# Optimization experiments

Measured on AMD Instinct MI355X. Metric: run time of the kernel, lower is better.

Reference implementation:

```python
import jax, jax.numpy as jnp
import numpy as np

B, I, O, G = 4096, 256, 256, 8
GRID_MIN, GRID_MAX, RHO = -2.0, 2.0, 1.0


def setup_inputs() -> dict:
    key = jax.random.key(0)
    ks = jax.random.split(key, 8)
    return {
        "x_re": jax.random.normal(ks[0], (B, I), dtype=jnp.float32),
        "x_im": jax.random.normal(ks[1], (B, I), dtype=jnp.float32),
        "realweights": jax.random.normal(ks[2], (I, O, G, G), dtype=jnp.float32),
        "complexweights": jax.random.normal(ks[3], (I, O, G, G), dtype=jnp.float32),
        "silu_weight_re": jax.random.normal(ks[4], (I, O), dtype=jnp.float32),
        "silu_weight_im": jax.random.normal(ks[5], (I, O), dtype=jnp.float32),
        "silu_bias_re": 0.1 * jax.random.normal(ks[6], (I, O), dtype=jnp.float32),
        "silu_bias_im": 0.1 * jax.random.normal(ks[7], (I, O), dtype=jnp.float32),
    }


def reference(x_re, x_im, realweights, complexweights,
              silu_weight_re, silu_weight_im, silu_bias_re, silu_bias_im):
    # Complex grid: grid[u, v] = lin[u] + i * lin[v]
    lin = jnp.linspace(GRID_MIN, GRID_MAX, G, dtype=x_re.dtype)
    # |x - grid|^2 = (x_re - lin_u)^2 + (x_im - lin_v)^2  -> (B, I, G, G)
    dre = x_re[:, :, None, None] - lin[None, None, :, None]
    dim = x_im[:, :, None, None] - lin[None, None, None, :]
    basis = jnp.exp(-(dre * dre + dim * dim) / RHO)  # real-valued (B, I, G, G)
    # RBF contraction: real and imaginary output channels
    out_re = jnp.einsum('biuv,iouv->bo', basis, realweights)
    out_im = jnp.einsum('biuv,iouv->bo', basis, complexweights)
    # Complex SiLU (complex_weight variant): silu applied component-wise,
    # then complex-multiplied by silu_weight, plus bias, summed over i.
    s_re = jax.nn.silu(x_re)  # (B, I)
    s_im = jax.nn.silu(x_im)
    out_re = out_re + s_re @ silu_weight_re - s_im @ silu_weight_im + jnp.sum(silu_bias_re, axis=0)
    out_im = out_im + s_im @ silu_weight_re + s_re @ silu_weight_im + jnp.sum(silu_bias_im, axis=0)
    # Return complex output as stacked (real, imag): (B, O, 2)
    return jnp.stack([out_re, out_im], axis=-1)
```

## Files before the change

### kernel.cpp

```cpp
#include <hip/hip_runtime.h>
#include <stdint.h>

typedef float floatx4 __attribute__((ext_vector_type(4)));
typedef _Float16 half8 __attribute__((ext_vector_type(8)));
typedef _Float16 half2t __attribute__((ext_vector_type(2)));

constexpr int I_SZ = 256, O_SZ = 256, NCOL = 512, B_SZ = 4096;
constexpr int KSTEPS = 264;
constexpr float GSTEP = 4.0f / 7.0f;
constexpr float NLOG2E = -1.44269504088896f;

__device__ __forceinline__ float silu_f(float a) {
  return a * __builtin_amdgcn_rcpf(1.f + __builtin_amdgcn_exp2f(a * NLOG2E));
}
__device__ __forceinline__ void gload_lds16(const void* g, void* l) {
  __builtin_amdgcn_global_load_lds((const __attribute__((address_space(1))) void*)g,
                                   (__attribute__((address_space(3))) void*)l,
                                   16, 0, 0);
}

union H8 { half8 v; half2t h[4]; uint32_t u[4]; };

__global__ void prelude(const float* __restrict__ rw, const float* __restrict__ cw,
                        const float* __restrict__ swre, const float* __restrict__ swim,
                        const float* __restrict__ bre, const float* __restrict__ bim,
                        const float* __restrict__ xre, const float* __restrict__ xim,
                        _Float16* __restrict__ wpack, float* __restrict__ bsum,
                        _Float16* __restrict__ eivT, _Float16* __restrict__ erqT,
                        _Float16* __restrict__ sTab, float* __restrict__ out) {
  __shared__ float tileR[64][65];
  __shared__ float tileI[64][65];
  const int bid = blockIdx.x, tid = threadIdx.x;

  if (bid < 4224) {
    int idx = bid * 256 + tid;
    int kb = idx >> 12;
    int rem = idx & 4095;
    int n = rem >> 3, gp = rem & 7;
    int g = gp ^ (n & 7);
    int o = n >> 1, c = n & 1;
    float w[8];
    if (kb < 256) {
      const float* W = (c ? cw : rw) + (((size_t)kb * O_SZ + o) << 6) + (g << 3);
      float4 a = *(const float4*)W;
      float4 b = *(const float4*)(W + 4);
      w[0] = a.x; w[1] = a.y; w[2] = a.z; w[3] = a.w;
      w[4] = b.x; w[5] = b.y; w[6] = b.z; w[7] = b.w;
    } else {
      int kp0 = ((kb - 256) << 6) + (g << 3);
      #pragma unroll
      for (int e = 0; e < 8; ++e) {
        int kp = kp0 + e, i = kp >> 1, ci = kp & 1;
        float a = swre[i * O_SZ + o], b = swim[i * O_SZ + o];
        w[e] = (c == 0) ? (ci == 0 ? a : -b) : (ci == 0 ? b : a);
      }
    }
    H8 val;
    #pragma unroll
    for (int e = 0; e < 8; ++e) val.v[e] = (_Float16)w[e];
    *(H8*)(wpack + (size_t)idx * 8) = val;
  } else if (bid < 4480) {
    int tb = bid - 4224;
    int bt = tb & 63, it = tb >> 6;
    int b0 = bt << 6, i0 = it << 6;
    int il = tid & 63, bh = tid >> 6;
    #pragma unroll
    for (int k = 0; k < 16; ++k) {
      int bl = bh + (k << 2);
      tileR[bl][il] = xre[(size_t)(b0 + bl) * I_SZ + i0 + il];
      tileI[bl][il] = xim[(size_t)(b0 + bl) * I_SZ + i0 + il];
    }
    __syncthreads();
    #pragma unroll
    for (int k = 0; k < 16; ++k) {
      int p = k * 256 + tid;
      int i_l = p >> 6, b_l = p & 63;
      float xr = tileR[b_l][i_l];
      float xi = tileI[b_l][i_l];
      float eru[8], eiv[8];
      #pragma unroll
      for (int g = 0; g < 8; ++g) {
        float dr = xr - (-2.0f + g * GSTEP);
        float di = xi - (-2.0f + g * GSTEP);
        eru[g] = __builtin_amdgcn_exp2f(dr * dr * NLOG2E);
        eiv[g] = __builtin_amdgcn_exp2f(di * di * NLOG2E);
      }
      size_t base = ((size_t)(i0 + i_l) * B_SZ + b0 + b_l) * 8;
      H8 ev, eq;
      #pragma unroll
      for (int g = 0; g < 8; ++g) ev.v[g] = (_Float16)eiv[g];
      #pragma unroll
      for (int q = 0; q < 4; ++q) { eq.v[2 * q] = (_Float16)eru[q]; eq.v[2 * q + 1] = (_Float16)eru[q + 4]; }
      *(H8*)(eivT + base) = ev;
      *(H8*)(erqT + base) = eq;
    }
  } else if (bid < 4992) {
    int tg = (bid - 4480) * 256 + tid;
    int b = tg >> 5, io = (tg & 31) << 3;
    const float* pr = xre + (size_t)b * I_SZ + io;
    const float* pi = xim + (size_t)b * I_SZ + io;
    float4 r0 = *(const float4*)pr, r1 = *(const float4*)(pr + 4);
    float4 q0 = *(const float4*)pi, q1 = *(const float4*)(pi + 4);
    H8 lo, hi;
    lo.v[0] = (_Float16)silu_f(r0.x); lo.v[1] = (_Float16)silu_f(q0.x);
    lo.v[2] = (_Float16)silu_f(r0.y); lo.v[3] = (_Float16)silu_f(q0.y);
    lo.v[4] = (_Float16)silu_f(r0.z); lo.v[5] = (_Float16)silu_f(q0.z);
    lo.v[6] = (_Float16)silu_f(r0.w); lo.v[7] = (_Float16)silu_f(q0.w);
    hi.v[0] = (_Float16)silu_f(r1.x); hi.v[1] = (_Float16)silu_f(q1.x);
    hi.v[2] = (_Float16)silu_f(r1.y); hi.v[3] = (_Float16)silu_f(q1.y);
    hi.v[4] = (_Float16)silu_f(r1.z); hi.v[5] = (_Float16)silu_f(q1.z);
    hi.v[6] = (_Float16)silu_f(r1.w); hi.v[7] = (_Float16)silu_f(q1.w);
    _Float16* dst = sTab + (size_t)b * 512 + 2 * io;
    *(H8*)dst = lo;
    *(H8*)(dst + 8) = hi;
  } else if (bid < 5120) {
    int w = tid >> 6, l = tid & 63;
    int n = (bid - 4992) * 4 + w;
    int o = n >> 1;
    const float* src = ((n & 1) ? bim : bre) + o;
    float s = 0.f;
    #pragma unroll
    for (int a = 0; a < 4; ++a) s += src[(size_t)(a * 64 + l) * O_SZ];
    #pragma unroll
    for (int off = 32; off; off >>= 1) s += __shfl_down(s, off, 64);
    if (l == 0) bsum[n] = s;
  } else {
    int z = bid - 5120;
    float4* o4 = (float4*)out;
    float4 zv = {0.f, 0.f, 0.f, 0.f};
    #pragma unroll
    for (int k = 0; k < 4; ++k) o4[(size_t)z * 1024 + k * 256 + tid] = zv;
  }
}

__global__ __launch_bounds__(256, 2) void cvkan_gemm(
    const _Float16* __restrict__ eivT, const _Float16* __restrict__ erqT,
    const _Float16* __restrict__ sTab,
    const _Float16* __restrict__ wpack, const float* __restrict__ bsum,
    float* __restrict__ out) {
  __shared__ __align__(16) _Float16 Bs[2][64 * 64];

  const int tid = threadIdx.x, bid = blockIdx.x;
  const int kch = bid & 7;
  const int rest = bid >> 3;
  const int mt = rest & 7, nt = rest >> 3;
  const int b0 = mt * 512, n0 = nt * 64;
  const int w = tid >> 6, l = tid & 63;
  const int lm = l & 15, q = l >> 4;
  const int row0 = b0 + w * 128 + lm;

  floatx4 acc[8][4] = {};

  {
    const _Float16* slab = wpack + ((size_t)(kch * 32) * NCOL + n0) * 64 + (w << 10) + (l << 3);
    _Float16* dst = &Bs[0][0] + (w << 10);
    gload_lds16(slab, dst);
    gload_lds16(slab + 512, dst + 512);
  }

  for (int j = 0; j < 33; ++j) {
    const int s = (j < 32) ? (kch * 32 + j) : (256 + kch);

    __syncthreads();

    half8 eivr[8]; half2t erqr[8];
    half8 afs[8][2];
    if (j < 32) {
      #pragma unroll
      for (int mm = 0; mm < 8; ++mm) {
        size_t base = ((size_t)s * B_SZ + row0 + mm * 16) * 8;
        eivr[mm] = *(const half8*)(eivT + base);
        erqr[mm] = *(const half2t*)(erqT + base + (q << 1));
      }
    } else {
      #pragma unroll
      for (int mm = 0; mm < 8; ++mm) {
        const _Float16* p = sTab + (size_t)(row0 + mm * 16) * 512 + kch * 64 + (q << 3);
        afs[mm][0] = *(const half8*)p;
        afs[mm][1] = *(const half8*)(p + 32);
      }
    }

    if (j < 32) {
      const int s1 = (j < 31) ? (s + 1) : (256 + kch);
      const _Float16* slab = wpack + ((size_t)s1 * NCOL + n0) * 64 + (w << 10) + (l << 3);
      _Float16* dst = &Bs[(j + 1) & 1][0] + (w << 10);
      gload_lds16(slab, dst);
      gload_lds16(slab + 512, dst + 512);
    }

    half8 bf[4][2];
    const _Float16* bp0 = &Bs[j & 1][0];
    #pragma unroll
    for (int nn = 0; nn < 4; ++nn) {
      int c = nn * 16 + lm;
      const _Float16* bp = bp0 + (c << 6);
      bf[nn][0] = *(const half8*)(bp + ((q       ^ (c & 7)) << 3));
      bf[nn][1] = *(const half8*)(bp + (((q + 4) ^ (c & 7)) << 3));
    }

    #pragma unroll
    for (int mm = 0; mm < 8; ++mm) {
      half8 a0, a1;
      if (j < 32) {
        H8 ev; ev.v = eivr[mm];
        half2t e0 = {erqr[mm].x, erqr[mm].x};
        half2t e1 = {erqr[mm].y, erqr[mm].y};
        H8 r0, r1;
        #pragma unroll
        for (int t = 0; t < 4; ++t) { r0.h[t] = e0 * ev.h[t]; r1.h[t] = e1 * ev.h[t]; }
        a0 = r0.v; a1 = r1.v;
      } else {
        a0 = afs[mm][0]; a1 = afs[mm][1];
      }
      #pragma unroll
      for (int nn = 0; nn < 4; ++nn) {
        acc[mm][nn] = __builtin_amdgcn_mfma_f32_16x16x32_f16(a0, bf[nn][0], acc[mm][nn], 0, 0, 0);
        acc[mm][nn] = __builtin_amdgcn_mfma_f32_16x16x32_f16(a1, bf[nn][1], acc[mm][nn], 0, 0, 0);
      }
    }
  }

  #pragma unroll
  for (int nn = 0; nn < 4; ++nn) {
    int col = n0 + nn * 16 + lm;
    float bv = (kch == 7) ? bsum[col] : 0.0f;
    #pragma unroll
    for (int mm = 0; mm < 8; ++mm) {
      int r0 = b0 + w * 128 + mm * 16 + (q << 2);
      #pragma unroll
      for (int r2 = 0; r2 < 4; ++r2)
        atomicAdd(out + (size_t)(r0 + r2) * NCOL + col, acc[mm][nn][r2] + bv);
    }
  }
}

extern "C" void kernel_launch(void* const* d_in, const int* in_sizes, int n_in,
                              void* d_out, int out_size, void* d_ws, size_t ws_size,
                              hipStream_t stream) {
  const float* xre  = (const float*)d_in[0];
  const float* xim  = (const float*)d_in[1];
  const float* rw   = (const float*)d_in[2];
  const float* cw   = (const float*)d_in[3];
  const float* swre = (const float*)d_in[4];
  const float* swim = (const float*)d_in[5];
  const float* bre  = (const float*)d_in[6];
  const float* bim  = (const float*)d_in[7];
  float* out = (float*)d_out;

  size_t off = 0;
  _Float16* wpack = (_Float16*)((char*)d_ws + off); off += (size_t)KSTEPS * NCOL * 64 * 2;
  _Float16* eivT  = (_Float16*)((char*)d_ws + off); off += (size_t)I_SZ * B_SZ * 8 * 2;
  _Float16* erqT  = (_Float16*)((char*)d_ws + off); off += (size_t)I_SZ * B_SZ * 8 * 2;
  _Float16* sTab  = (_Float16*)((char*)d_ws + off); off += (size_t)B_SZ * 512 * 2;
  float*    bsum  = (float*)((char*)d_ws + off);

  prelude<<<5632, 256, 0, stream>>>(rw, cw, swre, swim, bre, bim, xre, xim,
                                    wpack, bsum, eivT, erqT, sTab, out);
  cvkan_gemm<<<512, 256, 0, stream>>>(eivT, erqT, sTab, wpack, bsum, out);
}
```

Measured before the change: 233.0 us.

## Software-pipeline A-table register loads one step ahead of MFMA compute

Restructures the K loop into a two-step unrolled pipeline. The eiv/erq A-operand tables for the next step are loaded into registers while the current step's MFMAs run, alongside the existing LDS double-buffering of B. The j<32 branching inside the loop is removed and the SiLU table step is peeled into an epilogue. The aim is to hide global-load latency on A, at the cost of doubled A registers, which may pressure occupancy under launch_bounds(256,2).

```diff
diff --git a/kernel.cpp b/kernel.cpp
--- a/kernel.cpp
+++ b/kernel.cpp
@@ -151,72 +151,85 @@
 
   floatx4 acc[8][4] = {};
 
-  {
-    const _Float16* slab = wpack + ((size_t)(kch * 32) * NCOL + n0) * 64 + (w << 10) + (l << 3);
-    _Float16* dst = &Bs[0][0] + (w << 10);
+  auto stageB = [&](int s, int buf) {
+    const _Float16* slab = wpack + ((size_t)s * NCOL + n0) * 64 + (w << 10) + (l << 3);
+    _Float16* dst = &Bs[buf][0] + (w << 10);
     gload_lds16(slab, dst);
     gload_lds16(slab + 512, dst + 512);
-  }
-
-  for (int j = 0; j < 33; ++j) {
-    const int s = (j < 32) ? (kch * 32 + j) : (256 + kch);
-
-    __syncthreads();
-
-    half8 eivr[8]; half2t erqr[8];
-    half8 afs[8][2];
-    if (j < 32) {
-      #pragma unroll
-      for (int mm = 0; mm < 8; ++mm) {
-        size_t base = ((size_t)s * B_SZ + row0 + mm * 16) * 8;
-        eivr[mm] = *(const half8*)(eivT + base);
-        erqr[mm] = *(const half2t*)(erqT + base + (q << 1));
-      }
-    } else {
-      #pragma unroll
-      for (int mm = 0; mm < 8; ++mm) {
-        const _Float16* p = sTab + (size_t)(row0 + mm * 16) * 512 + kch * 64 + (q << 3);
-        afs[mm][0] = *(const half8*)p;
-        afs[mm][1] = *(const half8*)(p + 32);
-      }
-    }
-
-    if (j < 32) {
-      const int s1 = (j < 31) ? (s + 1) : (256 + kch);
-      const _Float16* slab = wpack + ((size_t)s1 * NCOL + n0) * 64 + (w << 10) + (l << 3);
-      _Float16* dst = &Bs[(j + 1) & 1][0] + (w << 10);
-      gload_lds16(slab, dst);
-      gload_lds16(slab + 512, dst + 512);
-    }
-
-    half8 bf[4][2];
-    const _Float16* bp0 = &Bs[j & 1][0];
+  };
+  auto loadTabs = [&](int s, half8* eiv, half2t* erq) {
+    #pragma unroll
+    for (int mm = 0; mm < 8; ++mm) {
+      size_t base = ((size_t)s * B_SZ + row0 + mm * 16) * 8;
+      eiv[mm] = *(const half8*)(eivT + base);
+      erq[mm] = *(const half2t*)(erqT + base + (q << 1));
+    }
+  };
+  auto compute = [&](int buf, const half8* eiv, const half2t* erq) {
+    half8 bf0[4], bf1[4];
+    const _Float16* bp0 = &Bs[buf][0];
     #pragma unroll
     for (int nn = 0; nn < 4; ++nn) {
       int c = nn * 16 + lm;
       const _Float16* bp = bp0 + (c << 6);
-      bf[nn][0] = *(const half8*)(bp + ((q       ^ (c & 7)) << 3));
-      bf[nn][1] = *(const half8*)(bp + (((q + 4) ^ (c & 7)) << 3));
-    }
-
-    #pragma unroll
-    for (int mm = 0; mm < 8; ++mm) {
-      half8 a0, a1;
-      if (j < 32) {
-        H8 ev; ev.v = eivr[mm];
-        half2t e0 = {erqr[mm].x, erqr[mm].x};
-        half2t e1 = {erqr[mm].y, erqr[mm].y};
-        H8 r0, r1;
-        #pragma unroll
-        for (int t = 0; t < 4; ++t) { r0.h[t] = e0 * ev.h[t]; r1.h[t] = e1 * ev.h[t]; }
-        a0 = r0.v; a1 = r1.v;
-      } else {
-        a0 = afs[mm][0]; a1 = afs[mm][1];
-      }
+      bf0[nn] = *(const half8*)(bp + ((q       ^ (c & 7)) << 3));
+      bf1[nn] = *(const half8*)(bp + (((q + 4) ^ (c & 7)) << 3));
+    }
+    #pragma unroll
+    for (int mm = 0; mm < 8; ++mm) {
+      H8 ev; ev.v = eiv[mm];
+      half2t e0 = {erq[mm].x, erq[mm].x};
+      half2t e1 = {erq[mm].y, erq[mm].y};
+      H8 r0, r1;
+      #pragma unroll
+      for (int t = 0; t < 4; ++t) { r0.h[t] = e0 * ev.h[t]; r1.h[t] = e1 * ev.h[t]; }
       #pragma unroll
       for (int nn = 0; nn < 4; ++nn) {
-        acc[mm][nn] = __builtin_amdgcn_mfma_f32_16x16x32_f16(a0, bf[nn][0], acc[mm][nn], 0, 0, 0);
-        acc[mm][nn] = __builtin_amdgcn_mfma_f32_16x16x32_f16(a1, bf[nn][1], acc[mm][nn], 0, 0, 0);
+        acc[mm][nn] = __builtin_amdgcn_mfma_f32_16x16x32_f16(r0.v, bf0[nn], acc[mm][nn], 0, 0, 0);
+        acc[mm][nn] = __builtin_amdgcn_mfma_f32_16x16x32_f16(r1.v, bf1[nn], acc[mm][nn], 0, 0, 0);
+      }
+    }
+  };
+
+  half8 eivC[8], eivN[8];
+  half2t erqC[8], erqN[8];
+
+  stageB(kch * 32, 0);
+  loadTabs(kch * 32, eivC, erqC);
+
+  #pragma unroll 1
+  for (int jj = 0; jj < 16; ++jj) {
+    const int s0 = kch * 32 + 2 * jj;
+    __syncthreads();
+    stageB(s0 + 1, 1);
+    loadTabs(s0 + 1, eivN, erqN);
+    compute(0, eivC, erqC);
+    __syncthreads();
+    if (jj < 15) { stageB(s0 + 2, 0); loadTabs(s0 + 2, eivC, erqC); }
+    else         { stageB(256 + kch, 0); }
+    compute(1, eivN, erqN);
+  }
+
+  __syncthreads();
+  {
+    half8 bf0[4], bf1[4];
+    const _Float16* bp0 = &Bs[0][0];
+    #pragma unroll
+    for (int nn = 0; nn < 4; ++nn) {
+      int c = nn * 16 + lm;
+      const _Float16* bp = bp0 + (c << 6);
+      bf0[nn] = *(const half8*)(bp + ((q       ^ (c & 7)) << 3));
+      bf1[nn] = *(const half8*)(bp + (((q + 4) ^ (c & 7)) << 3));
+    }
+    #pragma unroll
+    for (int mm = 0; mm < 8; ++mm) {
+      const _Float16* p = sTab + (size_t)(row0 + mm * 16) * 512 + kch * 64 + (q << 3);
+      half8 a0 = *(const half8*)p;
+      half8 a1 = *(const half8*)(p + 32);
+      #pragma unroll
+      for (int nn = 0; nn < 4; ++nn) {
+        acc[mm][nn] = __builtin_amdgcn_mfma_f32_16x16x32_f16(a0, bf0[nn], acc[mm][nn], 0, 0, 0);
+        acc[mm][nn] = __builtin_amdgcn_mfma_f32_16x16x32_f16(a1, bf1[nn], acc[mm][nn], 0, 0, 0);
       }
     }
   }
```

New measurement: 228.9 us. About the same (-1.7%).

## Halve GEMM M-tile, fuse SiLU into GEMM, replace atomics with split-K reduce

Applied to the files above, without the earlier changes.

The GEMM M-tile shrinks from 512 to 256 rows, so the grid doubles to 1024 blocks, accumulator registers halve, and launch bounds rise to 3 blocks per CU for more parallelism and occupancy. The SiLU table precompute is removed from the prelude and SiLU is computed inline from x in the final K step. When the workspace is large enough, per-K-chunk partial sums go to a buffer and a separate reduce kernel adds them with the bias, replacing the atomicAdd epilogue. This adds an extra kernel launch and a large write and read of 8 partial tiles to remove atomic contention and the zeroing pass.

```diff
diff --git a/kernel.cpp b/kernel.cpp
--- a/kernel.cpp
+++ b/kernel.cpp
@@ -9,6 +9,7 @@
 constexpr int KSTEPS = 264;
 constexpr float GSTEP = 4.0f / 7.0f;
 constexpr float NLOG2E = -1.44269504088896f;
+constexpr size_t PART_STRIDE = (size_t)B_SZ * NCOL;
 
 __device__ __forceinline__ float silu_f(float a) {
   return a * __builtin_amdgcn_rcpf(1.f + __builtin_amdgcn_exp2f(a * NLOG2E));
@@ -27,7 +28,7 @@
                         const float* __restrict__ xre, const float* __restrict__ xim,
                         _Float16* __restrict__ wpack, float* __restrict__ bsum,
                         _Float16* __restrict__ eivT, _Float16* __restrict__ erqT,
-                        _Float16* __restrict__ sTab, float* __restrict__ out) {
+                        float* __restrict__ out) {
   __shared__ float tileR[64][65];
   __shared__ float tileI[64][65];
   const int bid = blockIdx.x, tid = threadIdx.x;
@@ -94,28 +95,9 @@
       *(H8*)(eivT + base) = ev;
       *(H8*)(erqT + base) = eq;
     }
-  } else if (bid < 4992) {
-    int tg = (bid - 4480) * 256 + tid;
-    int b = tg >> 5, io = (tg & 31) << 3;
-    const float* pr = xre + (size_t)b * I_SZ + io;
-    const float* pi = xim + (size_t)b * I_SZ + io;
-    float4 r0 = *(const float4*)pr, r1 = *(const float4*)(pr + 4);
-    float4 q0 = *(const float4*)pi, q1 = *(const float4*)(pi + 4);
-    H8 lo, hi;
-    lo.v[0] = (_Float16)silu_f(r0.x); lo.v[1] = (_Float16)silu_f(q0.x);
-    lo.v[2] = (_Float16)silu_f(r0.y); lo.v[3] = (_Float16)silu_f(q0.y);
-    lo.v[4] = (_Float16)silu_f(r0.z); lo.v[5] = (_Float16)silu_f(q0.z);
-    lo.v[6] = (_Float16)silu_f(r0.w); lo.v[7] = (_Float16)silu_f(q0.w);
-    hi.v[0] = (_Float16)silu_f(r1.x); hi.v[1] = (_Float16)silu_f(q1.x);
-    hi.v[2] = (_Float16)silu_f(r1.y); hi.v[3] = (_Float16)silu_f(q1.y);
-    hi.v[4] = (_Float16)silu_f(r1.z); hi.v[5] = (_Float16)silu_f(q1.z);
-    hi.v[6] = (_Float16)silu_f(r1.w); hi.v[7] = (_Float16)silu_f(q1.w);
-    _Float16* dst = sTab + (size_t)b * 512 + 2 * io;
-    *(H8*)dst = lo;
-    *(H8*)(dst + 8) = hi;
-  } else if (bid < 5120) {
+  } else if (bid < 4608) {
     int w = tid >> 6, l = tid & 63;
-    int n = (bid - 4992) * 4 + w;
+    int n = (bid - 4480) * 4 + w;
     int o = n >> 1;
     const float* src = ((n & 1) ? bim : bre) + o;
     float s = 0.f;
@@ -125,7 +107,7 @@
     for (int off = 32; off; off >>= 1) s += __shfl_down(s, off, 64);
     if (l == 0) bsum[n] = s;
   } else {
-    int z = bid - 5120;
+    int z = bid - 4608;
     float4* o4 = (float4*)out;
     float4 zv = {0.f, 0.f, 0.f, 0.f};
     #pragma unroll
@@ -133,74 +115,80 @@
   }
 }
 
-__global__ __launch_bounds__(256, 2) void cvkan_gemm(
+__global__ __launch_bounds__(256, 3) void cvkan_gemm(
     const _Float16* __restrict__ eivT, const _Float16* __restrict__ erqT,
-    const _Float16* __restrict__ sTab,
+    const float* __restrict__ xre, const float* __restrict__ xim,
     const _Float16* __restrict__ wpack, const float* __restrict__ bsum,
-    float* __restrict__ out) {
+    float* __restrict__ part, float* __restrict__ out, int use_split) {
   __shared__ __align__(16) _Float16 Bs[2][64 * 64];
 
   const int tid = threadIdx.x, bid = blockIdx.x;
   const int kch = bid & 7;
   const int rest = bid >> 3;
-  const int mt = rest & 7, nt = rest >> 3;
-  const int b0 = mt * 512, n0 = nt * 64;
+  const int mt = rest & 15, nt = rest >> 4;
+  const int b0 = mt * 256, n0 = nt * 64;
   const int w = tid >> 6, l = tid & 63;
   const int lm = l & 15, q = l >> 4;
-  const int row0 = b0 + w * 128 + lm;
-
-  floatx4 acc[8][4] = {};
-
-  {
-    const _Float16* slab = wpack + ((size_t)(kch * 32) * NCOL + n0) * 64 + (w << 10) + (l << 3);
-    _Float16* dst = &Bs[0][0] + (w << 10);
+  const int row0 = b0 + w * 64 + lm;
+
+  floatx4 acc[4][4] = {};
+
+  auto stageB = [&](int s, int buf) {
+    const _Float16* slab = wpack + ((size_t)s * NCOL + n0) * 64 + (w << 10) + (l << 3);
+    _Float16* dst = &Bs[buf][0] + (w << 10);
     gload_lds16(slab, dst);
     gload_lds16(slab + 512, dst + 512);
-  }
+  };
+
+  stageB(kch * 32, 0);
 
   for (int j = 0; j < 33; ++j) {
     const int s = (j < 32) ? (kch * 32 + j) : (256 + kch);
 
     __syncthreads();
 
-    half8 eivr[8]; half2t erqr[8];
-    half8 afs[8][2];
+    half8 eivr[4]; half2t erqr[4];
+    half8 afs[4][2];
     if (j < 32) {
       #pragma unroll
-      for (int mm = 0; mm < 8; ++mm) {
+      for (int mm = 0; mm < 4; ++mm) {
         size_t base = ((size_t)s * B_SZ + row0 + mm * 16) * 8;
         eivr[mm] = *(const half8*)(eivT + base);
         erqr[mm] = *(const half2t*)(erqT + base + (q << 1));
       }
     } else {
       #pragma unroll
-      for (int mm = 0; mm < 8; ++mm) {
-        const _Float16* p = sTab + (size_t)(row0 + mm * 16) * 512 + kch * 64 + (q << 3);
-        afs[mm][0] = *(const half8*)p;
-        afs[mm][1] = *(const half8*)(p + 32);
-      }
-    }
-
-    if (j < 32) {
-      const int s1 = (j < 31) ? (s + 1) : (256 + kch);
-      const _Float16* slab = wpack + ((size_t)s1 * NCOL + n0) * 64 + (w << 10) + (l << 3);
-      _Float16* dst = &Bs[(j + 1) & 1][0] + (w << 10);
-      gload_lds16(slab, dst);
-      gload_lds16(slab + 512, dst + 512);
-    }
-
-    half8 bf[4][2];
+      for (int mm = 0; mm < 4; ++mm) {
+        const int row = row0 + mm * 16;
+        #pragma unroll
+        for (int kh = 0; kh < 2; ++kh) {
+          int i0 = kch * 32 + (q + kh * 4) * 4;
+          float4 fr = *(const float4*)(xre + (size_t)row * I_SZ + i0);
+          float4 fi = *(const float4*)(xim + (size_t)row * I_SZ + i0);
+          H8 a;
+          a.v[0] = (_Float16)silu_f(fr.x); a.v[1] = (_Float16)silu_f(fi.x);
+          a.v[2] = (_Float16)silu_f(fr.y); a.v[3] = (_Float16)silu_f(fi.y);
+          a.v[4] = (_Float16)silu_f(fr.z); a.v[5] = (_Float16)silu_f(fi.z);
+          a.v[6] = (_Float16)silu_f(fr.w); a.v[7] = (_Float16)silu_f(fi.w);
+          afs[mm][kh] = a.v;
+        }
+      }
+    }
+
+    if (j < 32) stageB((j < 31) ? (s + 1) : (256 + kch), (j + 1) & 1);
+
+    half8 bf0[4], bf1[4];
     const _Float16* bp0 = &Bs[j & 1][0];
     #pragma unroll
     for (int nn = 0; nn < 4; ++nn) {
       int c = nn * 16 + lm;
       const _Float16* bp = bp0 + (c << 6);
-      bf[nn][0] = *(const half8*)(bp + ((q       ^ (c & 7)) << 3));
-      bf[nn][1] = *(const half8*)(bp + (((q + 4) ^ (c & 7)) << 3));
-    }
-
-    #pragma unroll
-    for (int mm = 0; mm < 8; ++mm) {
+      bf0[nn] = *(const half8*)(bp + ((q       ^ (c & 7)) << 3));
+      bf1[nn] = *(const half8*)(bp + (((q + 4) ^ (c & 7)) << 3));
+    }
+
+    #pragma unroll
+    for (int mm = 0; mm < 4; ++mm) {
       half8 a0, a1;
       if (j < 32) {
         H8 ev; ev.v = eivr[mm];
@@ -215,24 +203,53 @@
       }
       #pragma unroll
       for (int nn = 0; nn < 4; ++nn) {
-        acc[mm][nn] = __builtin_amdgcn_mfma_f32_16x16x32_f16(a0, bf[nn][0], acc[mm][nn], 0, 0, 0);
-        acc[mm][nn] = __builtin_amdgcn_mfma_f32_16x16x32_f16(a1, bf[nn][1], acc[mm][nn], 0, 0, 0);
-      }
-    }
-  }
-
+        acc[mm][nn] = __builtin_amdgcn_mfma_f32_16x16x32_f16(a0, bf0[nn], acc[mm][nn], 0, 0, 0);
+        acc[mm][nn] = __builtin_amdgcn_mfma_f32_16x16x32_f16(a1, bf1[nn], acc[mm][nn], 0, 0, 0);
+      }
+    }
+  }
+
+  if (use_split) {
+    float* dst = part + (size_t)kch * PART_STRIDE;
+    #pragma unroll
+    for (int nn = 0; nn < 4; ++nn) {
+      int col = n0 + nn * 16 + lm;
+      #pragma unroll
+      for (int mm = 0; mm < 4; ++mm) {
+        int r0 = b0 + w * 64 + mm * 16 + (q << 2);
+        #pragma unroll
+        for (int r2 = 0; r2 < 4; ++r2)
+          dst[(size_t)(r0 + r2) * NCOL + col] = acc[mm][nn][r2];
+      }
+    }
+  } else {
+    #pragma unroll
+    for (int nn = 0; nn < 4; ++nn) {
+      int col = n0 + nn * 16 + lm;
+      float bv = (kch == 7) ? bsum[col] : 0.0f;
+      #pragma unroll
+      for (int mm = 0; mm < 4; ++mm) {
+        int r0 = b0 + w * 64 + mm * 16 + (q << 2);
+        #pragma unroll
+        for (int r2 = 0; r2 < 4; ++r2)
+          atomicAdd(out + (size_t)(r0 + r2) * NCOL + col, acc[mm][nn][r2] + bv);
+      }
+    }
+  }
+}
+
+__global__ void reduce_k(const float* __restrict__ part, const float* __restrict__ bsum,
+                         float* __restrict__ out) {
+  size_t idx4 = (size_t)blockIdx.x * 256 + threadIdx.x;
+  size_t base = idx4 * 4;
+  int n = (int)(base & (NCOL - 1));
+  float4 s = *(const float4*)(bsum + n);
   #pragma unroll
-  for (int nn = 0; nn < 4; ++nn) {
-    int col = n0 + nn * 16 + lm;
-    float bv = (kch == 7) ? bsum[col] : 0.0f;
-    #pragma unroll
-    for (int mm = 0; mm < 8; ++mm) {
-      int r0 = b0 + w * 128 + mm * 16 + (q << 2);
-      #pragma unroll
-      for (int r2 = 0; r2 < 4; ++r2)
-        atomicAdd(out + (size_t)(r0 + r2) * NCOL + col, acc[mm][nn][r2] + bv);
-    }
-  }
+  for (int k = 0; k < 8; ++k) {
+    float4 p = *(const float4*)(part + k * PART_STRIDE + base);
+    s.x += p.x; s.y += p.y; s.z += p.z; s.w += p.w;
+  }
+  *(float4*)(out + base) = s;
 }
 
 extern "C" void kernel_launch(void* const* d_in, const int* in_sizes, int n_in,
@@ -252,10 +269,17 @@
   _Float16* wpack = (_Float16*)((char*)d_ws + off); off += (size_t)KSTEPS * NCOL * 64 * 2;
   _Float16* eivT  = (_Float16*)((char*)d_ws + off); off += (size_t)I_SZ * B_SZ * 8 * 2;
   _Float16* erqT  = (_Float16*)((char*)d_ws + off); off += (size_t)I_SZ * B_SZ * 8 * 2;
-  _Float16* sTab  = (_Float16*)((char*)d_ws + off); off += (size_t)B_SZ * 512 * 2;
-  float*    bsum  = (float*)((char*)d_ws + off);
-
-  prelude<<<5632, 256, 0, stream>>>(rw, cw, swre, swim, bre, bim, xre, xim,
-                                    wpack, bsum, eivT, erqT, sTab, out);
-  cvkan_gemm<<<512, 256, 0, stream>>>(eivT, erqT, sTab, wpack, bsum, out);
-}
+  float*    part  = (float*)((char*)d_ws + off);
+  size_t part_bytes = 8 * PART_STRIDE * sizeof(float);
+  size_t need_split = off + part_bytes + NCOL * sizeof(float);
+  const bool use_split = (ws_size >= need_split);
+  float* bsum = use_split ? (float*)((char*)d_ws + off + part_bytes)
+                          : (float*)((char*)d_ws + off);
+
+  prelude<<<use_split ? 4608 : 5120, 256, 0, stream>>>(
+      rw, cw, swre, swim, bre, bim, xre, xim, wpack, bsum, eivT, erqT, out);
+  cvkan_gemm<<<1024, 256, 0, stream>>>(eivT, erqT, xre, xim, wpack, bsum,
+                                       part, out, (int)use_split);
+  if (use_split)
+    reduce_k<<<2048, 256, 0, stream>>>(part, bsum, out);
+}
```

Result: faster. 216.6 us (-7.0%).
